# Kernel tuning notes

Measured on AMD Instinct MI355X. Metric: run time of the kernel, lower is better.

The kernel has to match this reference:

```python
import jax, jax.numpy as jnp
import numpy as np
from jax import lax

VOL = (128, 192, 192)
PATCH = (64, 64, 64)
DOWN = (4, 4, 4)
C = 8
STRIDE = 32


def gaussian_importance_map(patch_size, sigma_scale=0.125):
    # MONAI-style separable gaussian centered at size//2, sigma = size*sigma_scale,
    # normalized to max 1, zero values clamped to smallest positive value.
    axes = []
    for s in patch_size:
        center = s // 2
        sigma = sigma_scale * s
        x = jnp.arange(s, dtype=jnp.float32)
        axes.append(jnp.exp(-0.5 * ((x - center) / sigma) ** 2))
    w = axes[0][:, None, None] * axes[1][None, :, None] * axes[2][None, None, :]
    w = w / w.max()
    pos_min = jnp.min(jnp.where(w > 0, w, jnp.inf))
    return jnp.maximum(w, pos_min)  # [Hp, Wp, Dp]


def make_grid_starts():
    zs = np.arange(0, VOL[0] - PATCH[0] + 1, STRIDE)
    ys = np.arange(0, VOL[1] - PATCH[1] + 1, STRIDE)
    xs = np.arange(0, VOL[2] - PATCH[2] + 1, STRIDE)
    g = np.stack(np.meshgrid(zs, ys, xs, indexing='ij'), axis=-1).reshape(-1, 3)
    return jnp.asarray(g, dtype=jnp.int32)  # [75, 3]


def setup_inputs() -> dict:
    key = jax.random.key(0)
    k1, k2 = jax.random.split(key)
    starts = make_grid_starts()
    n = starts.shape[0]
    logit_patches = jax.random.normal(k1, (n, C) + PATCH, dtype=jnp.float32)
    hg, wg, dg = (VOL[0] // DOWN[0], VOL[1] // DOWN[1], VOL[2] // DOWN[2])
    global_logit = jax.random.normal(k2, (1, C, hg, wg, dg), dtype=jnp.float32)
    return {"logit_patches": logit_patches, "global_logit": global_logit, "starts": starts}


def reference(logit_patches, global_logit, starts):
    wt = gaussian_importance_map(PATCH)[None, None]  # [1,1,Hp,Wp,Dp]

    # trilinear upsample (align_corners=False semantics, half-pixel centers)
    up_global = jax.image.resize(global_logit, (1, C) + VOL, method='trilinear')

    final_logit = jnp.zeros((1, C) + VOL, dtype=jnp.float32)
    weight_map = jnp.full((1, 1) + VOL, 1e-20, dtype=jnp.float32)
    mask = jnp.zeros((1, 1) + VOL, dtype=jnp.float32)
    ones_patch = jnp.ones((1, 1) + PATCH, dtype=jnp.float32)

    def body(carry, inp):
        fl, wm, mk = carry
        patch, st = inp
        idx5 = (0, 0, st[0], st[1], st[2])
        cur = lax.dynamic_slice(fl, idx5, (1, C) + PATCH)
        fl = lax.dynamic_update_slice(fl, cur + patch[None] * wt, idx5)
        curw = lax.dynamic_slice(wm, idx5, (1, 1) + PATCH)
        wm = lax.dynamic_update_slice(wm, curw + wt, idx5)
        mk = lax.dynamic_update_slice(mk, ones_patch, idx5)
        return (fl, wm, mk), None

    (final_logit, weight_map, mask), _ = lax.scan(
        body, (final_logit, weight_map, mask), (logit_patches, starts))

    final_logit = final_logit / weight_map
    final_logit = final_logit + jnp.where(mask == 1.0, 0.0, up_global)
    return final_logit
```

## Files before the change

kernel.cpp:

```cpp
#include <hip/hip_runtime.h>

#define VZ 128
#define VY 192
#define VX 192
#define NC 8
#define PS 64
#define PS3 (PS * PS * PS)

typedef float f4 __attribute__((ext_vector_type(4)));

__global__ __launch_bounds__(256)
void agg_kernel(const float* __restrict__ patches, float* __restrict__ out)
{
    __shared__ float g[PS];
    const int t = threadIdx.y * 8 + threadIdx.x;
    if (t < PS) {
        const float d = ((float)t - 32.0f) * 0.125f;
        g[t] = __expf(-0.5f * d * d);
    }
    __syncthreads();

    const int bx = blockIdx.x % 6;
    const int by = blockIdx.x / 6;
    const int x0 = bx * 32 + (threadIdx.x << 2);
    const int y  = by * 32 + threadIdx.y;
    const int z  = blockIdx.y;
    const int c0 = blockIdx.z << 1;

    const int szh = min(64, (z >> 5) << 5);
    const int szl = szh - 32;
    const bool z2 = (z >= 32) & (z < 96);
    const int syh = min(128, by * 32);
    const int syl = syh - 32;
    const bool y2 = (by >= 1) & (by <= 4);
    const int sxh = min(128, bx * 32);
    const int sxl = sxh - 32;
    const bool x2 = (bx >= 1) & (bx <= 4);

    const f4* g4 = (const f4*)g;
    const f4 wxh = g4[(x0 - sxh) >> 2];
    f4 wxl = {0.f, 0.f, 0.f, 0.f};
    if (x2) wxl = g4[(x0 - sxl) >> 2];
    const float gzh = g[z - szh];
    const float gyh = g[y - syh];
    const float gzl = z2 ? g[z - szl] : 0.0f;
    const float gyl = y2 ? g[y - syl] : 0.0f;

    f4 acc0 = {0.f, 0.f, 0.f, 0.f};
    f4 acc1 = {0.f, 0.f, 0.f, 0.f};
    f4 wsum = {1e-20f, 1e-20f, 1e-20f, 1e-20f};

#define PROC(SZ, SY, SX, WZY, WX)                                              \
    do {                                                                       \
        const int p = (((SZ) >> 5) * 5 + ((SY) >> 5)) * 5 + ((SX) >> 5);       \
        const size_t base = ((size_t)(p * NC + c0)) * PS3 +                    \
            (((size_t)(z - (SZ)) * PS + (size_t)(y - (SY))) * PS) +            \
            (size_t)(x0 - (SX));                                               \
        const f4 cw = (WZY) * (WX);                                            \
        wsum += cw;                                                            \
        const f4 pv0 = __builtin_nontemporal_load((const f4*)(patches + base));\
        const f4 pv1 = __builtin_nontemporal_load(                             \
            (const f4*)(patches + base + PS3));                                \
        acc0 += pv0 * cw;                                                      \
        acc1 += pv1 * cw;                                                      \
    } while (0)

    PROC(szh, syh, sxh, gzh * gyh, wxh);
    if (x2) PROC(szh, syh, sxl, gzh * gyh, wxl);
    if (y2) {
        PROC(szh, syl, sxh, gzh * gyl, wxh);
        if (x2) PROC(szh, syl, sxl, gzh * gyl, wxl);
    }
    if (z2) {
        PROC(szl, syh, sxh, gzl * gyh, wxh);
        if (x2) PROC(szl, syh, sxl, gzl * gyh, wxl);
        if (y2) {
            PROC(szl, syl, sxh, gzl * gyl, wxh);
            if (x2) PROC(szl, syl, sxl, gzl * gyl, wxl);
        }
    }
#undef PROC

    f4 inv;
    inv.x = __builtin_amdgcn_rcpf(wsum.x);
    inv.y = __builtin_amdgcn_rcpf(wsum.y);
    inv.z = __builtin_amdgcn_rcpf(wsum.z);
    inv.w = __builtin_amdgcn_rcpf(wsum.w);

    const size_t ob = (((size_t)c0 * VZ + z) * VY + y) * VX + x0;
    __builtin_nontemporal_store(acc0 * inv, (f4*)(out + ob));
    __builtin_nontemporal_store(acc1 * inv,
                                (f4*)(out + ob + (size_t)VZ * VY * VX));
}

extern "C" void kernel_launch(void* const* d_in, const int* in_sizes, int n_in,
                              void* d_out, int out_size, void* d_ws, size_t ws_size,
                              hipStream_t stream) {
    const float* patches = (const float*)d_in[0];
    float* out = (float*)d_out;

    dim3 block(8, 32, 1);
    dim3 grid(6 * 6, VZ, NC / 2);
    agg_kernel<<<grid, block, 0, stream>>>(patches, out);
}
```

Baseline: 148.8 us.

## Retile blocks to 64-wide x spans aligned with full patch rows

Blocks become 16x16 threads covering 64 consecutive x voxels that line up with one patch's full x extent. Each thread always reads from that patch and, when needed, from the half-overlapping neighbour patch via a fixed pointer delta. This replaces the per-32-wide x-tile branching. The goal is fewer divergent branches and more uniform, contiguous 256-byte row loads per wavefront. The half-patch path still diverges between the two halves of a wavefront.

```diff
diff --git a/kernel.cpp b/kernel.cpp
--- a/kernel.cpp
+++ b/kernel.cpp
@@ -13,71 +13,76 @@
 void agg_kernel(const float* __restrict__ patches, float* __restrict__ out)
 {
     __shared__ float g[PS];
-    const int t = threadIdx.y * 8 + threadIdx.x;
+    const int tx = threadIdx.x;
+    const int ty = threadIdx.y;
+    const int t = ty * 16 + tx;
     if (t < PS) {
         const float d = ((float)t - 32.0f) * 0.125f;
         g[t] = __expf(-0.5f * d * d);
     }
     __syncthreads();
 
-    const int bx = blockIdx.x % 6;
-    const int by = blockIdx.x / 6;
-    const int x0 = bx * 32 + (threadIdx.x << 2);
-    const int y  = by * 32 + threadIdx.y;
-    const int z  = blockIdx.y;
-    const int c0 = blockIdx.z << 1;
+    const int xt = blockIdx.x % 3;
+    const int yt = blockIdx.x / 3;
+    const int X = xt * 64, Y = yt * 16;
+    const int z = blockIdx.y;
+    const int c0 = blockIdx.z * 2;
+
+    const int y = Y + ty;
 
     const int szh = min(64, (z >> 5) << 5);
-    const int szl = szh - 32;
     const bool z2 = (z >= 32) & (z < 96);
-    const int syh = min(128, by * 32);
-    const int syl = syh - 32;
-    const bool y2 = (by >= 1) & (by <= 4);
-    const int sxh = min(128, bx * 32);
-    const int sxl = sxh - 32;
-    const bool x2 = (bx >= 1) & (bx <= 4);
+    const int syh = min(128, (Y >> 5) << 5);
+    const bool y2 = (syh >= 32) && ((Y - syh) < 32);
+    const int pxf = X >> 5;
+
+    const bool hasHalf = (tx < 8) ? (xt >= 1) : (xt <= 1);
+    const long hDelta = (tx < 8) ? (-(long)(NC * PS3) + 32)
+                                 : ((long)(NC * PS3) - 32);
 
     const f4* g4 = (const f4*)g;
-    const f4 wxh = g4[(x0 - sxh) >> 2];
-    f4 wxl = {0.f, 0.f, 0.f, 0.f};
-    if (x2) wxl = g4[(x0 - sxl) >> 2];
+    const f4 wxf = g4[tx];
+    const f4 wxh = g4[tx ^ 8];
+
     const float gzh = g[z - szh];
     const float gyh = g[y - syh];
-    const float gzl = z2 ? g[z - szl] : 0.0f;
-    const float gyl = y2 ? g[y - syl] : 0.0f;
+    const float gzl = z2 ? g[z - szh + 32] : 0.0f;
+    const float gyl = y2 ? g[y - syh + 32] : 0.0f;
 
     f4 acc0 = {0.f, 0.f, 0.f, 0.f};
     f4 acc1 = {0.f, 0.f, 0.f, 0.f};
     f4 wsum = {1e-20f, 1e-20f, 1e-20f, 1e-20f};
 
-#define PROC(SZ, SY, SX, WZY, WX)                                              \
+#define PROC(SZ, SY, GZY)                                                      \
     do {                                                                       \
-        const int p = (((SZ) >> 5) * 5 + ((SY) >> 5)) * 5 + ((SX) >> 5);       \
-        const size_t base = ((size_t)(p * NC + c0)) * PS3 +                    \
+        const int p = ((SZ) >> 5) * 25 + ((SY) >> 5) * 5 + pxf;                \
+        const size_t offf = ((size_t)(p * NC + c0)) * PS3 +                    \
             (((size_t)(z - (SZ)) * PS + (size_t)(y - (SY))) * PS) +            \
-            (size_t)(x0 - (SX));                                               \
-        const f4 cw = (WZY) * (WX);                                            \
-        wsum += cw;                                                            \
-        const f4 pv0 = __builtin_nontemporal_load((const f4*)(patches + base));\
-        const f4 pv1 = __builtin_nontemporal_load(                             \
-            (const f4*)(patches + base + PS3));                                \
-        acc0 += pv0 * cw;                                                      \
-        acc1 += pv1 * cw;                                                      \
+            (size_t)(tx * 4);                                                  \
+        const float wzy = (GZY);                                               \
+        const f4 cwf = wzy * wxf;                                              \
+        wsum += cwf;                                                           \
+        const f4 av = __builtin_nontemporal_load((const f4*)(patches + offf)); \
+        const f4 bv = __builtin_nontemporal_load(                              \
+            (const f4*)(patches + offf + PS3));                                \
+        acc0 += av * cwf;                                                      \
+        acc1 += bv * cwf;                                                      \
+        if (hasHalf) {                                                         \
+            const f4 cwh = wzy * wxh;                                          \
+            wsum += cwh;                                                       \
+            const float* ph = patches + (long)offf + hDelta;                   \
+            const f4 ah = __builtin_nontemporal_load((const f4*)ph);           \
+            const f4 bh = __builtin_nontemporal_load((const f4*)(ph + PS3));   \
+            acc0 += ah * cwh;                                                  \
+            acc1 += bh * cwh;                                                  \
+        }                                                                      \
     } while (0)
 
-    PROC(szh, syh, sxh, gzh * gyh, wxh);
-    if (x2) PROC(szh, syh, sxl, gzh * gyh, wxl);
-    if (y2) {
-        PROC(szh, syl, sxh, gzh * gyl, wxh);
-        if (x2) PROC(szh, syl, sxl, gzh * gyl, wxl);
-    }
+    PROC(szh, syh, gzh * gyh);
+    if (y2) PROC(szh, syh - 32, gzh * gyl);
     if (z2) {
-        PROC(szl, syh, sxh, gzl * gyh, wxh);
-        if (x2) PROC(szl, syh, sxl, gzl * gyh, wxl);
-        if (y2) {
-            PROC(szl, syl, sxh, gzl * gyl, wxh);
-            if (x2) PROC(szl, syl, sxl, gzl * gyl, wxl);
-        }
+        PROC(szh - 32, syh, gzl * gyh);
+        if (y2) PROC(szh - 32, syh - 32, gzl * gyl);
     }
 #undef PROC
 
@@ -87,7 +92,7 @@
     inv.z = __builtin_amdgcn_rcpf(wsum.z);
     inv.w = __builtin_amdgcn_rcpf(wsum.w);
 
-    const size_t ob = (((size_t)c0 * VZ + z) * VY + y) * VX + x0;
+    const size_t ob = (((size_t)c0 * VZ + z) * VY + y) * VX + (size_t)(X + tx * 4);
     __builtin_nontemporal_store(acc0 * inv, (f4*)(out + ob));
     __builtin_nontemporal_store(acc1 * inv,
                                 (f4*)(out + ob + (size_t)VZ * VY * VX));
@@ -99,7 +104,7 @@
     const float* patches = (const float*)d_in[0];
     float* out = (float*)d_out;
 
-    dim3 block(8, 32, 1);
-    dim3 grid(6 * 6, VZ, NC / 2);
+    dim3 block(16, 16, 1);
+    dim3 grid(3 * 12, VZ, NC / 2);
     agg_kernel<<<grid, block, 0, stream>>>(patches, out);
 }
```

New measurement: 145.7 us. 1.02x faster.
